# Performance work log

Measured on AMD Instinct MI355X. Metric: run time of the kernel, lower is better.

The kernel has to match this reference:

```python
import jax, jax.numpy as jnp
import numpy as np

NUM_STEPS = 151            # num_steps from __init__
STEP = 2.0 / (NUM_STEPS - 1)
HALF = (NUM_STEPS - 1) // 2  # bin offset: t_j = -1 + j*STEP, 1/STEP = HALF
N = 4096
D = 512
NUM_CLASSES = 751


def _soft_histogram(s, mask, size):
    # Triangular-kernel (linear) soft binning, equivalent to the original
    # indsa/indsb masked-repeat construction: each similarity s in
    # [t_{j-1}, t_j] contributes (1-frac) to bin j-1 and frac to bin j.
    x = s / STEP
    k = jnp.floor(x)           # zero-gradient, plays the role of s_repeat_floor
    frac = x - k               # (s - (t_j - STEP)) / STEP
    kI = k.astype(jnp.int32)
    idx_lo = jnp.clip(kI + HALF, 0, NUM_STEPS - 1)
    idx_hi = jnp.clip(kI + HALF + 1, 0, NUM_STEPS - 1)
    hist = jnp.zeros((NUM_STEPS,), dtype=s.dtype)
    hist = hist.at[idx_lo].add((1.0 - frac) * mask)
    hist = hist.at[idx_hi].add(frac * mask)
    return hist / size


def setup_inputs() -> dict:
    key = jax.random.key(0)
    kf, kc = jax.random.split(key)
    return {
        "features": jax.random.normal(kf, (N, D), dtype=jnp.float32),
        "classes": jax.random.randint(kc, (N,), 0, NUM_CLASSES, dtype=jnp.int32),
    }


def reference(features, classes):
    # L2Normalization
    f = features / jnp.linalg.norm(features, axis=1, keepdims=True)
    dists = f @ f.T                                   # [N, N] cosine sims
    iu, ju = np.triu_indices(features.shape[0], 1)    # static upper-tri pairs
    s = dists[iu, ju]                                 # [P] P = N(N-1)/2
    pos = (classes[iu] == classes[ju]).astype(s.dtype)
    neg = 1.0 - pos
    hist_pos = _soft_histogram(s, pos, jnp.sum(pos))
    hist_neg = _soft_histogram(s, neg, jnp.sum(neg))
    cdf_pos = jnp.cumsum(hist_pos)                    # tril-masked column sums == cumsum
    return jnp.sum(hist_neg * cdf_pos)
```

## Files before the change

kernel.cpp:

```cpp
#include <hip/hip_runtime.h>
#include <math.h>

#define N 4096
#define D 512
#define NUM_STEPS 151
#define HALF_BINS 75
#define INV_STEP 75.0f
#define NUM_CLASSES 751
#define P_TOTAL 8386560.0f

#define WS_SUM_ALL 0
#define WS_POS_CNT 1
#define WS_SUM_POS 2
#define WS_S_POS   3
#define WS_G_OFF   8
#define WS_LIST_OFF 1024
#define MAXP (1 << 18)
#define WS_FEAT_OFF (WS_LIST_OFF + MAXP)
#define WS_FEATB_OFF (WS_FEAT_OFF + N * D)
#define WS_IDX_OFF  (WS_FEATB_OFF + N * D / 2)
#define WS_OFFS_OFF (WS_IDX_OFF + N)
#define WS_POFF_OFF (WS_OFFS_OFF + NUM_CLASSES + 1)

typedef __bf16 bf16x8 __attribute__((ext_vector_type(8)));
typedef float floatx4 __attribute__((ext_vector_type(4)));

__global__ __launch_bounds__(256) void k_normalize(const float* __restrict__ feat,
                                                   float* __restrict__ nf,
                                                   __bf16* __restrict__ nfb) {
    int row = blockIdx.x;
    int t = threadIdx.x;
    const float* fr = feat + (size_t)row * D;
    float a = fr[t];
    float b = fr[t + 256];
    float ss = a * a + b * b;
    for (int o = 32; o > 0; o >>= 1) ss += __shfl_down(ss, o, 64);
    __shared__ float wsum[4];
    int lane = t & 63, wid = t >> 6;
    if (lane == 0) wsum[wid] = ss;
    __syncthreads();
    float tot = wsum[0] + wsum[1] + wsum[2] + wsum[3];
    float inv = 1.0f / sqrtf(tot);
    float na = a * inv, nb = b * inv;
    nf[(size_t)row * D + t] = na;
    nf[(size_t)row * D + t + 256] = nb;
    nfb[(size_t)row * D + t] = (__bf16)na;
    nfb[(size_t)row * D + t + 256] = (__bf16)nb;
}

__global__ __launch_bounds__(256) void k_sort(const int* __restrict__ cls,
                                              int* __restrict__ rowIdx,
                                              int* __restrict__ offs,
                                              int* __restrict__ pairOffs,
                                              int* __restrict__ posCntOut) {
    __shared__ int hcnt[NUM_CLASSES];
    __shared__ int hoff[NUM_CLASSES];
    __shared__ int poff[NUM_CLASSES];
    __shared__ int wsumR[4], wsumP[4];
    int t = threadIdx.x;
    for (int c = t; c < NUM_CLASSES; c += 256) hcnt[c] = 0;
    __syncthreads();
    for (int n = t; n < N; n += 256) atomicAdd(&hcnt[cls[n]], 1);
    __syncthreads();

    int c0 = t * 3;
    int cntPreR[3], cntPreP[3];
    int myR = 0, myP = 0;
    #pragma unroll
    for (int k = 0; k < 3; ++k) {
        int c = c0 + k;
        int cnt = (c < NUM_CLASSES) ? hcnt[c] : 0;
        cntPreR[k] = myR; cntPreP[k] = myP;
        myR += cnt;
        myP += cnt * (cnt - 1) / 2;
    }
    int lane = t & 63, wv = t >> 6;
    int incR = myR, incP = myP;
    for (int o = 1; o < 64; o <<= 1) {
        int rr = __shfl_up(incR, o, 64);
        int pp = __shfl_up(incP, o, 64);
        if (lane >= o) { incR += rr; incP += pp; }
    }
    if (lane == 63) { wsumR[wv] = incR; wsumP[wv] = incP; }
    __syncthreads();
    int baseR = 0, baseP = 0;
    for (int w = 0; w < wv; ++w) { baseR += wsumR[w]; baseP += wsumP[w]; }
    int exR = baseR + incR - myR;
    int exP = baseP + incP - myP;
    #pragma unroll
    for (int k = 0; k < 3; ++k) {
        int c = c0 + k;
        if (c < NUM_CLASSES) { hoff[c] = exR + cntPreR[k]; poff[c] = exP + cntPreP[k]; }
    }
    __syncthreads();

    for (int c = t; c < NUM_CLASSES; c += 256) hcnt[c] = hoff[c];
    __syncthreads();
    for (int n = t; n < N; n += 256) {
        int p = atomicAdd(&hcnt[cls[n]], 1);
        rowIdx[p] = n;
    }
    for (int c = t; c < NUM_CLASSES; c += 256) { offs[c] = hoff[c]; pairOffs[c] = poff[c]; }
    if (t == 0) {
        int totR = wsumR[0] + wsumR[1] + wsumR[2] + wsumR[3];
        int totP = wsumP[0] + wsumP[1] + wsumP[2] + wsumP[3];
        offs[NUM_CLASSES] = totR;
        pairOffs[NUM_CLASSES] = totP;
        *posCntOut = totP;
    }
}

__global__ __launch_bounds__(256) void k_pospairs3(const float* __restrict__ nf,
                                                   const int* __restrict__ rowIdx,
                                                   const int* __restrict__ offs,
                                                   const int* __restrict__ pairOffs,
                                                   float* __restrict__ posS) {
    int c = blockIdx.x;
    int o0 = offs[c], o1 = offs[c + 1];
    int nc = o1 - o0;
    if (nc < 2) return;
    int nPairs = nc * (nc - 1) / 2;
    int pBase = pairOffs[c];
    int lane = threadIdx.x & 63;
    int wave = threadIdx.x >> 6;
    for (int p = wave; p < nPairs; p += 4) {
        int a = 0, rem = p;
        while (rem >= nc - 1 - a) { rem -= nc - 1 - a; ++a; }
        int b = a + 1 + rem;
        int ri = rowIdx[o0 + a], rj = rowIdx[o0 + b];
        const float4* x4 = (const float4*)(nf + (size_t)ri * D);
        const float4* y4 = (const float4*)(nf + (size_t)rj * D);
        float4 xa = x4[lane * 2], xb = x4[lane * 2 + 1];
        float4 ya = y4[lane * 2], yb = y4[lane * 2 + 1];
        float s = xa.x * ya.x + xa.y * ya.y + xa.z * ya.z + xa.w * ya.w
                + xb.x * yb.x + xb.y * yb.y + xb.z * yb.z + xb.w * yb.w;
        for (int o = 32; o > 0; o >>= 1) s += __shfl_down(s, o, 64);
        if (lane == 0) posS[pBase + p] = s;
    }
}

__global__ __launch_bounds__(256) void k_build_cdf(const float* __restrict__ posS,
                                                   const int* __restrict__ posCnt,
                                                   float* __restrict__ G,
                                                   float* __restrict__ sumPosOut,
                                                   float* __restrict__ sPosOut) {
    __shared__ float hist[NUM_STEPS];
    __shared__ float Gs[NUM_STEPS];
    int t = threadIdx.x;
    int C = *posCnt;
    if (C > MAXP) C = MAXP;
    for (int b = t; b < NUM_STEPS; b += 256) hist[b] = 0.f;
    __syncthreads();
    for (int p = t; p < C; p += 256) {
        float s = posS[p];
        float x = s * INV_STEP;
        float kf = floorf(x);
        float frac = x - kf;
        int kI = (int)kf;
        int lo = min(max(kI + HALF_BINS, 0), NUM_STEPS - 1);
        int hi = min(max(kI + HALF_BINS + 1, 0), NUM_STEPS - 1);
        atomicAdd(&hist[lo], 1.0f - frac);
        atomicAdd(&hist[hi], frac);
    }
    __syncthreads();
    if (t == 0) {
        float invC = (C > 0) ? (1.0f / (float)C) : 0.f;
        float acc = 0.f;
        for (int b = 0; b < NUM_STEPS; ++b) {
            acc += hist[b];
            Gs[b] = acc * invC;
        }
    }
    __syncthreads();
    for (int b = t; b < NUM_STEPS; b += 256) G[b] = Gs[b];
    float ps = 0.f;
    for (int p = t; p < C; p += 256) {
        float s = posS[p];
        float x = s * INV_STEP;
        float kf = floorf(x);
        float frac = x - kf;
        int kI = (int)kf;
        int lo = min(max(kI + HALF_BINS, 0), NUM_STEPS - 1);
        int hi = min(max(kI + HALF_BINS + 1, 0), NUM_STEPS - 1);
        ps += (1.f - frac) * Gs[lo] + frac * Gs[hi];
    }
    for (int o = 32; o > 0; o >>= 1) ps += __shfl_down(ps, o, 64);
    __shared__ float wsum[4];
    int lane = t & 63, wid = t >> 6;
    if (lane == 0) wsum[wid] = ps;
    __syncthreads();
    if (t == 0) {
        *sumPosOut = wsum[0] + wsum[1] + wsum[2] + wsum[3];
        *sPosOut = (float)C;
    }
}

#define TILES_1D 32
#define LDSS 40

__global__ __launch_bounds__(256) void k_gram(const __bf16* __restrict__ nfb,
                                              const float* __restrict__ G,
                                              float* __restrict__ sumAll) {
    int bid = blockIdx.x;
    int ti = 0, rem = bid;
    while (rem >= TILES_1D - ti) { rem -= TILES_1D - ti; ++ti; }
    int tj = ti + rem;

    __shared__ __align__(16) __bf16 As[128 * LDSS];
    __shared__ __align__(16) __bf16 Bs[128 * LDSS];
    __shared__ float Gs[NUM_STEPS];

    int tid = threadIdx.x;
    for (int b = tid; b < NUM_STEPS; b += 256) Gs[b] = G[b];

    int lane = tid & 63;
    int wave = tid >> 6;
    int wm = (wave >> 1) * 64;
    int wn = (wave & 1) * 64;
    int fr = lane & 15;
    int fk = (lane >> 4) * 8;

    int rowA0 = ti * 128, rowB0 = tj * 128;

    floatx4 acc[4][4] = {};

    int e0 = tid * 8;
    int e1 = e0 + 2048;
    int r0 = e0 >> 5, c0 = e0 & 31;
    int r1 = e1 >> 5, c1 = e1 & 31;

    for (int kb = 0; kb < D / 32; ++kb) {
        int kbase = kb * 32;
        *(float4*)(&As[r0 * LDSS + c0]) = *(const float4*)(nfb + (size_t)(rowA0 + r0) * D + kbase + c0);
        *(float4*)(&As[r1 * LDSS + c1]) = *(const float4*)(nfb + (size_t)(rowA0 + r1) * D + kbase + c1);
        *(float4*)(&Bs[r0 * LDSS + c0]) = *(const float4*)(nfb + (size_t)(rowB0 + r0) * D + kbase + c0);
        *(float4*)(&Bs[r1 * LDSS + c1]) = *(const float4*)(nfb + (size_t)(rowB0 + r1) * D + kbase + c1);
        __syncthreads();

        bf16x8 a[4], b[4];
        #pragma unroll
        for (int r = 0; r < 4; ++r)
            a[r] = *(const bf16x8*)(&As[(wm + r * 16 + fr) * LDSS + fk]);
        #pragma unroll
        for (int c = 0; c < 4; ++c)
            b[c] = *(const bf16x8*)(&Bs[(wn + c * 16 + fr) * LDSS + fk]);

        #pragma unroll
        for (int r = 0; r < 4; ++r)
            #pragma unroll
            for (int c = 0; c < 4; ++c)
                acc[r][c] = __builtin_amdgcn_mfma_f32_16x16x32_bf16(a[r], b[c], acc[r][c], 0, 0, 0);
        __syncthreads();
    }

    int crow = (lane >> 4) * 4;
    int ccol = lane & 15;
    float gsum = 0.f;
    #pragma unroll
    for (int r = 0; r < 4; ++r) {
        #pragma unroll
        for (int c = 0; c < 4; ++c) {
            #pragma unroll
            for (int reg = 0; reg < 4; ++reg) {
                int gi = rowA0 + wm + r * 16 + crow + reg;
                int gj = rowB0 + wn + c * 16 + ccol;
                if (gi < gj) {
                    float s = acc[r][c][reg];
                    float x = s * INV_STEP;
                    float kf = floorf(x);
                    float frac = x - kf;
                    int kI = (int)kf;
                    int lo = min(max(kI + HALF_BINS, 0), NUM_STEPS - 1);
                    int hi = min(max(kI + HALF_BINS + 1, 0), NUM_STEPS - 1);
                    gsum += (1.f - frac) * Gs[lo] + frac * Gs[hi];
                }
            }
        }
    }
    for (int o = 32; o > 0; o >>= 1) gsum += __shfl_down(gsum, o, 64);
    __shared__ float wsum[4];
    if ((tid & 63) == 0) wsum[tid >> 6] = gsum;
    __syncthreads();
    if (tid == 0) atomicAdd(sumAll, wsum[0] + wsum[1] + wsum[2] + wsum[3]);
}

__global__ void k_final(const float* __restrict__ wsf, float* __restrict__ out) {
    float C = wsf[WS_S_POS];
    float sneg = P_TOTAL - C;
    out[0] = (wsf[WS_SUM_ALL] - wsf[WS_SUM_POS]) / sneg;
}

extern "C" void kernel_launch(void* const* d_in, const int* in_sizes, int n_in,
                              void* d_out, int out_size, void* d_ws, size_t ws_size,
                              hipStream_t stream) {
    const float* feat = (const float*)d_in[0];
    const int* cls = (const int*)d_in[1];
    float* out = (float*)d_out;
    float* wsf = (float*)d_ws;
    int* wsi = (int*)d_ws;

    hipMemsetAsync(d_ws, 0, 4096, stream);

    float* nf = wsf + WS_FEAT_OFF;
    __bf16* nfb = (__bf16*)(wsf + WS_FEATB_OFF);
    float* posS = wsf + WS_LIST_OFF;
    float* G = wsf + WS_G_OFF;
    int* rowIdx = wsi + WS_IDX_OFF;
    int* offs = wsi + WS_OFFS_OFF;
    int* pairOffs = wsi + WS_POFF_OFF;

    k_normalize<<<N, 256, 0, stream>>>(feat, nf, nfb);
    k_sort<<<1, 256, 0, stream>>>(cls, rowIdx, offs, pairOffs, wsi + WS_POS_CNT);
    k_pospairs3<<<NUM_CLASSES, 256, 0, stream>>>(nf, rowIdx, offs, pairOffs, posS);
    k_build_cdf<<<1, 256, 0, stream>>>(posS, wsi + WS_POS_CNT, G,
                                       wsf + WS_SUM_POS, wsf + WS_S_POS);
    int nTiles = TILES_1D * (TILES_1D + 1) / 2;
    k_gram<<<nTiles, 256, 0, stream>>>(nfb, G, wsf + WS_SUM_ALL);
    k_final<<<1, 1, 0, stream>>>(wsf, out);
}
```

Measured before the change: 159.8 us.

## Load gram tiles via direct global-to-LDS loads in MFMA-fragment layout

The gram kernel now loads bf16 tiles straight into LDS with global_load_lds, bypassing registers. Each wave writes 16x32 panels already arranged in MFMA fragment order, so a fragment read is one contiguous 16-byte access per lane and no padded layout is needed. The positive-pair kernel is also reduced from four waves to one wave per class, which cuts idle threads for the many small classes but serialises pairs within larger classes. The direct-to-LDS path relies on the builtin's ordering with respect to __syncthreads and on the new layout matching the fragment mapping.

```diff
diff --git a/kernel.cpp b/kernel.cpp
--- a/kernel.cpp
+++ b/kernel.cpp
@@ -24,6 +24,12 @@
 
 typedef __bf16 bf16x8 __attribute__((ext_vector_type(8)));
 typedef float floatx4 __attribute__((ext_vector_type(4)));
+
+__device__ __forceinline__ void load_lds16(const void* g, void* s) {
+    __builtin_amdgcn_global_load_lds(
+        (const __attribute__((address_space(1))) void*)g,
+        (__attribute__((address_space(3))) void*)s, 16, 0, 0);
+}
 
 __global__ __launch_bounds__(256) void k_normalize(const float* __restrict__ feat,
                                                    float* __restrict__ nf,
@@ -110,20 +116,19 @@
     }
 }
 
-__global__ __launch_bounds__(256) void k_pospairs3(const float* __restrict__ nf,
-                                                   const int* __restrict__ rowIdx,
-                                                   const int* __restrict__ offs,
-                                                   const int* __restrict__ pairOffs,
-                                                   float* __restrict__ posS) {
+__global__ __launch_bounds__(64) void k_pospairs3(const float* __restrict__ nf,
+                                                  const int* __restrict__ rowIdx,
+                                                  const int* __restrict__ offs,
+                                                  const int* __restrict__ pairOffs,
+                                                  float* __restrict__ posS) {
     int c = blockIdx.x;
     int o0 = offs[c], o1 = offs[c + 1];
     int nc = o1 - o0;
     if (nc < 2) return;
     int nPairs = nc * (nc - 1) / 2;
     int pBase = pairOffs[c];
-    int lane = threadIdx.x & 63;
-    int wave = threadIdx.x >> 6;
-    for (int p = wave; p < nPairs; p += 4) {
+    int lane = threadIdx.x;
+    for (int p = 0; p < nPairs; ++p) {
         int a = 0, rem = p;
         while (rem >= nc - 1 - a) { rem -= nc - 1 - a; ++a; }
         int b = a + 1 + rem;
@@ -196,7 +201,6 @@
 }
 
 #define TILES_1D 32
-#define LDSS 40
 
 __global__ __launch_bounds__(256) void k_gram(const __bf16* __restrict__ nfb,
                                               const float* __restrict__ G,
@@ -206,8 +210,8 @@
     while (rem >= TILES_1D - ti) { rem -= TILES_1D - ti; ++ti; }
     int tj = ti + rem;
 
-    __shared__ __align__(16) __bf16 As[128 * LDSS];
-    __shared__ __align__(16) __bf16 Bs[128 * LDSS];
+    __shared__ __align__(16) __bf16 As[8 * 512];
+    __shared__ __align__(16) __bf16 Bs[8 * 512];
     __shared__ float Gs[NUM_STEPS];
 
     int tid = threadIdx.x;
@@ -215,35 +219,39 @@
 
     int lane = tid & 63;
     int wave = tid >> 6;
-    int wm = (wave >> 1) * 64;
-    int wn = (wave & 1) * 64;
-    int fr = lane & 15;
-    int fk = (lane >> 4) * 8;
-
     int rowA0 = ti * 128, rowB0 = tj * 128;
 
+    int fr2 = lane & 15, kc2 = lane >> 4;
+    int pS0 = wave * 2, pS1 = wave * 2 + 1;
+    const __bf16* gA0 = nfb + (size_t)(rowA0 + pS0 * 16 + fr2) * D + kc2 * 8;
+    const __bf16* gA1 = nfb + (size_t)(rowA0 + pS1 * 16 + fr2) * D + kc2 * 8;
+    const __bf16* gB0 = nfb + (size_t)(rowB0 + pS0 * 16 + fr2) * D + kc2 * 8;
+    const __bf16* gB1 = nfb + (size_t)(rowB0 + pS1 * 16 + fr2) * D + kc2 * 8;
+    __bf16* lA0 = &As[pS0 * 512];
+    __bf16* lA1 = &As[pS1 * 512];
+    __bf16* lB0 = &Bs[pS0 * 512];
+    __bf16* lB1 = &Bs[pS1 * 512];
+
+    int pbA = (wave >> 1) * 4;
+    int pbB = (wave & 1) * 4;
+
     floatx4 acc[4][4] = {};
-
-    int e0 = tid * 8;
-    int e1 = e0 + 2048;
-    int r0 = e0 >> 5, c0 = e0 & 31;
-    int r1 = e1 >> 5, c1 = e1 & 31;
 
     for (int kb = 0; kb < D / 32; ++kb) {
         int kbase = kb * 32;
-        *(float4*)(&As[r0 * LDSS + c0]) = *(const float4*)(nfb + (size_t)(rowA0 + r0) * D + kbase + c0);
-        *(float4*)(&As[r1 * LDSS + c1]) = *(const float4*)(nfb + (size_t)(rowA0 + r1) * D + kbase + c1);
-        *(float4*)(&Bs[r0 * LDSS + c0]) = *(const float4*)(nfb + (size_t)(rowB0 + r0) * D + kbase + c0);
-        *(float4*)(&Bs[r1 * LDSS + c1]) = *(const float4*)(nfb + (size_t)(rowB0 + r1) * D + kbase + c1);
+        load_lds16(gA0 + kbase, lA0);
+        load_lds16(gA1 + kbase, lA1);
+        load_lds16(gB0 + kbase, lB0);
+        load_lds16(gB1 + kbase, lB1);
         __syncthreads();
 
         bf16x8 a[4], b[4];
         #pragma unroll
         for (int r = 0; r < 4; ++r)
-            a[r] = *(const bf16x8*)(&As[(wm + r * 16 + fr) * LDSS + fk]);
+            a[r] = *(const bf16x8*)(&As[(pbA + r) * 512 + lane * 8]);
         #pragma unroll
         for (int c = 0; c < 4; ++c)
-            b[c] = *(const bf16x8*)(&Bs[(wn + c * 16 + fr) * LDSS + fk]);
+            b[c] = *(const bf16x8*)(&Bs[(pbB + c) * 512 + lane * 8]);
 
         #pragma unroll
         for (int r = 0; r < 4; ++r)
@@ -255,6 +263,7 @@
 
     int crow = (lane >> 4) * 4;
     int ccol = lane & 15;
+    int wm = pbA * 16, wn = pbB * 16;
     float gsum = 0.f;
     #pragma unroll
     for (int r = 0; r < 4; ++r) {
@@ -311,7 +320,7 @@
 
     k_normalize<<<N, 256, 0, stream>>>(feat, nf, nfb);
     k_sort<<<1, 256, 0, stream>>>(cls, rowIdx, offs, pairOffs, wsi + WS_POS_CNT);
-    k_pospairs3<<<NUM_CLASSES, 256, 0, stream>>>(nf, rowIdx, offs, pairOffs, posS);
+    k_pospairs3<<<NUM_CLASSES, 64, 0, stream>>>(nf, rowIdx, offs, pairOffs, posS);
     k_build_cdf<<<1, 256, 0, stream>>>(posS, wsi + WS_POS_CNT, G,
                                        wsf + WS_SUM_POS, wsf + WS_S_POS);
     int nTiles = TILES_1D * (TILES_1D + 1) / 2;
```

Result: slower. 196.9 us (+23.2%).
